# Performance work log

Hardware: AMD Instinct MI355X
Metric: run time of the kernel (lower is better)

Reference implementation:

```python
import jax, jax.numpy as jnp
import numpy as np

KNN = 5            # module constant KNN
MAX_STEPS = 100    # laplacian_optimization default
BOUND_LAMBDA = 1.0 # laplacian_optimization default


def setup_inputs() -> dict:
    key = jax.random.key(0)
    k1, k2, k3 = jax.random.split(key, 3)
    N, D, C = 4096, 2048, 256
    x = jax.random.normal(k1, (N, D), dtype=jnp.float32)          # pooled backbone features
    W = jax.random.normal(k2, (C, D), dtype=jnp.float32) * 0.02   # classifier weight
    b = jax.random.normal(k3, (C,), dtype=jnp.float32) * 0.02     # classifier bias
    return {"x": x, "W": W, "b": b}


def _rbf_affinity(feats, knn):
    # pairwise euclidean distances via gram matrix (torch.cdist equivalent)
    sq = jnp.sum(feats * feats, axis=-1)
    d2 = jnp.maximum(sq[:, None] + sq[None, :] - 2.0 * (feats @ feats.T), 0.0)
    dist = jnp.sqrt(d2)
    # k-th smallest distance per row (self-distance included, matching torch.topk largest=False)
    kth = -jax.lax.top_k(-dist, knn)[0][:, -1]
    sigma = jnp.mean(kth)
    return jnp.exp(-d2 / (2.0 * sigma * sigma))


def _laplacian_optimization(unary, kernel):
    Y0 = jax.nn.softmax(-unary, axis=-1)

    def step(carry, i):
        Y, oldE, done = carry
        pairwise = BOUND_LAMBDA * (kernel @ Y)                      # [N,N]@[N,C]
        Ynew = jax.nn.softmax(-unary + pairwise, axis=-1)
        E = jnp.sum(unary * Ynew - BOUND_LAMBDA * pairwise * Ynew
                    + Ynew * jnp.log(jnp.clip(Ynew, 1e-20)))
        conv = (i > 1) & (jnp.abs(E - oldE) <= 1e-8 * jnp.abs(oldE))
        # freeze state after convergence (device-side analogue of the host .item() break)
        Yk = jnp.where(done, Y, Ynew)
        Ek = jnp.where(done, oldE, E)
        return (Yk, Ek, done | conv), None

    init = (Y0, jnp.array(jnp.inf, jnp.float32), jnp.array(False))
    (Y, _, _), _ = jax.lax.scan(step, init, jnp.arange(MAX_STEPS))
    return Y


def reference(x, W, b):
    logits = x @ W.T + b
    unary = -jnp.log(jax.nn.softmax(logits, axis=-1) + 1e-10)
    feats = x / jnp.linalg.norm(x, axis=-1, keepdims=True)          # F.normalize(p=2)
    kernel = _rbf_affinity(feats, KNN)
    return _laplacian_optimization(unary, kernel)
```

## Files before the change

kernel.cpp:

```cpp
#include <hip/hip_runtime.h>
#include <cstdint>

#define NP 4096
#define DIMF 2048
#define NC 256
#define MAXIT 100
#define NBLK2 256

typedef __bf16 bf16x8 __attribute__((ext_vector_type(8)));
typedef float f32x4 __attribute__((ext_vector_type(4)));

__device__ inline unsigned short f2b(float f) {
  union { float f; unsigned u; } v; v.f = f;
  unsigned r = v.u + 0x7fffu + ((v.u >> 16) & 1u);
  return (unsigned short)(r >> 16);
}
__device__ inline float b2f(unsigned short u) {
  union { unsigned u; float f; } v; v.u = ((unsigned)u) << 16;
  return v.f;
}

__device__ __forceinline__ void g2lds16(const void* g, void* l) {
  __builtin_amdgcn_global_load_lds(
      (const __attribute__((address_space(1))) unsigned int*)g,
      (__attribute__((address_space(3))) unsigned int*)l, 16, 0, 0);
}

__device__ __forceinline__ void gridbar(unsigned* flags, unsigned* gen,
                                        unsigned phase, int tid, int nblk) {
  __syncthreads();
  if (blockIdx.x == 0) {
    if (tid >= 1 && tid < nblk) {
      while (__hip_atomic_load(&flags[tid * 32], __ATOMIC_ACQUIRE,
                               __HIP_MEMORY_SCOPE_AGENT) < phase)
        __builtin_amdgcn_s_sleep(1);
    }
    __syncthreads();
    if (tid == 0)
      __hip_atomic_store(gen, phase, __ATOMIC_RELEASE, __HIP_MEMORY_SCOPE_AGENT);
  } else {
    if (tid == 0) {
      __hip_atomic_store(&flags[blockIdx.x * 32], phase, __ATOMIC_RELEASE,
                         __HIP_MEMORY_SCOPE_AGENT);
      while (__hip_atomic_load(gen, __ATOMIC_ACQUIRE,
                               __HIP_MEMORY_SCOPE_AGENT) < phase)
        __builtin_amdgcn_s_sleep(1);
    }
  }
  __syncthreads();
}

__global__ __launch_bounds__(256) void initk(double* Ed, float* sig,
                                             unsigned* flags, unsigned* gen) {
  int t = threadIdx.x;
  if (t < MAXIT) Ed[t] = 0.0;
  if (t == 0) { *sig = 0.0f; *gen = 0u; }
  for (int i = t; i < NBLK2 * 32; i += 256) flags[i] = 0u;
}

__global__ __launch_bounds__(256) void castk(const float* __restrict__ W,
                                             unsigned short* __restrict__ Wb) {
  size_t i = ((size_t)blockIdx.x * 256 + threadIdx.x) * 4;
  float4 v = *(const float4*)&W[i];
  ushort4 o; o.x = f2b(v.x); o.y = f2b(v.y); o.z = f2b(v.z); o.w = f2b(v.w);
  *(ushort4*)&Wb[i] = o;
}

__global__ __launch_bounds__(256) void rownorm(const float* __restrict__ x,
                                               unsigned short* __restrict__ F,
                                               unsigned short* __restrict__ xb,
                                               float* __restrict__ sqF) {
  const int row = blockIdx.x, tid = threadIdx.x;
  const float* rp = x + (size_t)row * DIMF;
  float4 a = *(const float4*)&rp[tid * 8];
  float4 b = *(const float4*)&rp[tid * 8 + 4];
  float f[8] = {a.x, a.y, a.z, a.w, b.x, b.y, b.z, b.w};
  float s = 0.f;
#pragma unroll
  for (int k = 0; k < 8; k++) s += f[k] * f[k];
  __shared__ float red[256];
  red[tid] = s; __syncthreads();
  for (int st = 128; st >= 1; st >>= 1) {
    if (tid < st) red[tid] += red[tid + st];
    __syncthreads();
  }
  float inv = 1.0f / sqrtf(red[0]);
  __syncthreads();
  unsigned short fb[8], xbv[8];
  float s2 = 0.f;
#pragma unroll
  for (int k = 0; k < 8; k++) {
    fb[k] = f2b(f[k] * inv);
    xbv[k] = f2b(f[k]);
    float q = b2f(fb[k]);
    s2 += q * q;
  }
  *(ushort4*)&F[(size_t)row * DIMF + tid * 8]      = *(ushort4*)&fb[0];
  *(ushort4*)&F[(size_t)row * DIMF + tid * 8 + 4]  = *(ushort4*)&fb[4];
  *(ushort4*)&xb[(size_t)row * DIMF + tid * 8]     = *(ushort4*)&xbv[0];
  *(ushort4*)&xb[(size_t)row * DIMF + tid * 8 + 4] = *(ushort4*)&xbv[4];
  red[tid] = s2; __syncthreads();
  for (int st = 128; st >= 1; st >>= 1) {
    if (tid < st) red[tid] += red[tid + st];
    __syncthreads();
  }
  if (tid == 0) sqF[row] = red[0];
}

template <int BM, int BN, int EPI>
__global__ __launch_bounds__(256) void gemm2(const unsigned short* __restrict__ A,
                                             const unsigned short* __restrict__ B,
                                             float* __restrict__ C,
                                             int M, int N, int K,
                                             const float* __restrict__ aux) {
  constexpr int TM = BM / 32, TN = BN / 32;
  __shared__ __align__(16) unsigned short sA[BM * 32];
  __shared__ __align__(16) unsigned short sB[BN * 32];
  const int tid = threadIdx.x, lane = tid & 63, wid = tid >> 6;
  const int wr = wid >> 1, wc = wid & 1;
  const int l15 = lane & 15, l16 = lane >> 4;
  const int bm = blockIdx.x * BM, bn = blockIdx.y * BN;
  f32x4 acc[TM][TN];
#pragma unroll
  for (int m = 0; m < TM; m++)
#pragma unroll
    for (int n = 0; n < TN; n++) acc[m][n] = 0.0f;

  for (int k0 = 0; k0 < K; k0 += 32) {
#pragma unroll
    for (int j = 0; j < BM / 64; ++j) {
      int u = j * 256 + tid, r = u >> 2, c = u & 3;
      g2lds16(&A[(size_t)(bm + r) * K + k0 + c * 8], &sA[u * 8]);
    }
#pragma unroll
    for (int j = 0; j < BN / 64; ++j) {
      int u = j * 256 + tid, r = u >> 2, c = u & 3;
      g2lds16(&B[(size_t)(bn + r) * K + k0 + c * 8], &sB[u * 8]);
    }
    __syncthreads();
    bf16x8 af[TM], bf[TN];
#pragma unroll
    for (int m = 0; m < TM; m++)
      af[m] = *(const bf16x8*)&sA[(wr * TM * 16 + m * 16 + l15) * 32 + l16 * 8];
#pragma unroll
    for (int n = 0; n < TN; n++)
      bf[n] = *(const bf16x8*)&sB[(wc * TN * 16 + n * 16 + l15) * 32 + l16 * 8];
#pragma unroll
    for (int m = 0; m < TM; m++)
#pragma unroll
      for (int n = 0; n < TN; n++)
        acc[m][n] = __builtin_amdgcn_mfma_f32_16x16x32_bf16(af[m], bf[n], acc[m][n], 0, 0, 0);
    __syncthreads();
  }
#pragma unroll
  for (int m = 0; m < TM; m++) {
    int row0 = bm + wr * TM * 16 + m * 16 + l16 * 4;
#pragma unroll
    for (int n = 0; n < TN; n++) {
      int col = bn + wc * TN * 16 + n * 16 + l15;
#pragma unroll
      for (int j = 0; j < 4; j++) {
        int row = row0 + j;
        float v = acc[m][n][j];
        if (EPI == 0) {
          C[(size_t)row * N + col] = v + aux[col];
        } else {
          float d = aux[row] + aux[col] - 2.0f * v;
          C[(size_t)row * N + col] = fmaxf(d, 0.0f);
        }
      }
    }
  }
}

__global__ __launch_bounds__(256) void unary_k(const float* __restrict__ logits,
                                               float* __restrict__ unary) {
  const int wid = threadIdx.x >> 6, lane = threadIdx.x & 63;
  const int row = blockIdx.x * 4 + wid;
  const float* lp = logits + (size_t)row * NC;
  float v[4];
#pragma unroll
  for (int j = 0; j < 4; j++) v[j] = lp[lane + 64 * j];
  float m = fmaxf(fmaxf(v[0], v[1]), fmaxf(v[2], v[3]));
#pragma unroll
  for (int o = 32; o >= 1; o >>= 1) m = fmaxf(m, __shfl_xor(m, o, 64));
  float e[4], s = 0.f;
#pragma unroll
  for (int j = 0; j < 4; j++) { e[j] = expf(v[j] - m); s += e[j]; }
#pragma unroll
  for (int o = 32; o >= 1; o >>= 1) s += __shfl_xor(s, o, 64);
  float* up = unary + (size_t)row * NC;
#pragma unroll
  for (int j = 0; j < 4; j++) up[lane + 64 * j] = -logf(e[j] / s + 1e-10f);
}


__global__ __launch_bounds__(256) void smax0(const float* __restrict__ unary,
                                             float* __restrict__ Yout,
                                             unsigned short* __restrict__ Yt) {
  const int tid = threadIdx.x;
  const int wid = tid >> 6, lane = tid & 63;
  const int rb = blockIdx.x;
  __shared__ __align__(16) unsigned short yt[256][24];
  for (int rr = wid; rr < 16; rr += 4) {
    const int row = rb * 16 + rr;
    float z[4];
#pragma unroll
    for (int j = 0; j < 4; j++) z[j] = -unary[(size_t)row * NC + lane + 64 * j];
    float m = fmaxf(fmaxf(z[0], z[1]), fmaxf(z[2], z[3]));
#pragma unroll
    for (int o = 32; o >= 1; o >>= 1) m = fmaxf(m, __shfl_xor(m, o, 64));
    float e[4], s = 0.f;
#pragma unroll
    for (int j = 0; j < 4; j++) { e[j] = expf(z[j] - m); s += e[j]; }
#pragma unroll
    for (int o = 32; o >= 1; o >>= 1) s += __shfl_xor(s, o, 64);
#pragma unroll
    for (int j = 0; j < 4; j++) {
      int c = lane + 64 * j;
      float y = e[j] / s;
      Yout[(size_t)row * NC + c] = y;
      yt[c][rr] = f2b(y);
    }
  }
  __syncthreads();
  const int c = tid;
#pragma unroll
  for (int r8 = 0; r8 < 2; ++r8) {
    unsigned v[4];
#pragma unroll
    for (int k = 0; k < 4; ++k) {
      unsigned lo = yt[c][r8 * 8 + 2 * k];
      unsigned hi = yt[c][r8 * 8 + 2 * k + 1];
      v[k] = lo | (hi << 16);
    }
    size_t off = ((size_t)(c >> 5) << 17) +
                 (size_t)(((rb * 2 + r8) * 32 + (c & 31)) * 8);
    *(uint4*)&Yt[off] = make_uint4(v[0], v[1], v[2], v[3]);
  }
}

__global__ __launch_bounds__(256) void kth_k(const float* __restrict__ d2,
                                             float* __restrict__ sig) {
  const int row = blockIdx.x, tid = threadIdx.x;
  const float* rp = d2 + (size_t)row * NP;
  float b[5];
#pragma unroll
  for (int q = 0; q < 5; q++) b[q] = __int_as_float(0x7f800000);
  for (int s = 0; s < 16; s++) {
    float v = rp[tid + 256 * s];
    if (v < b[4]) {
      b[4] = v;
#pragma unroll
      for (int q = 4; q > 0; q--)
        if (b[q] < b[q - 1]) { float t = b[q]; b[q] = b[q - 1]; b[q - 1] = t; }
    }
  }
  __shared__ float ls[256 * 5];
#pragma unroll
  for (int q = 0; q < 5; q++) ls[tid * 5 + q] = b[q];
  __syncthreads();
  for (int st = 128; st >= 1; st >>= 1) {
    if (tid < st) {
      float* xs = &ls[tid * 5];
      float* ys = &ls[(tid + st) * 5];
      float r[5]; int i = 0, j = 0;
#pragma unroll
      for (int q = 0; q < 5; q++) r[q] = (xs[i] <= ys[j]) ? xs[i++] : ys[j++];
#pragma unroll
      for (int q = 0; q < 5; q++) xs[q] = r[q];
    }
    __syncthreads();
  }
  if (tid == 0) atomicAdd(sig, sqrtf(ls[4]));
}

__global__ __launch_bounds__(256) void expk(const float* __restrict__ d2,
                                            unsigned short* __restrict__ Kb,
                                            const float* __restrict__ sig) {
  float sigma = (*sig) * (1.0f / NP);
  float c = -1.0f / (2.0f * sigma * sigma);
  size_t i = ((size_t)blockIdx.x * 256 + threadIdx.x) * 4;
  float4 v = *(const float4*)&d2[i];
  ushort4 o;
  o.x = f2b(expf(v.x * c)); o.y = f2b(expf(v.y * c));
  o.z = f2b(expf(v.z * c)); o.w = f2b(expf(v.w * c));
  *(ushort4*)&Kb[i] = o;
}

__global__ __launch_bounds__(512) void loop_k(const unsigned short* __restrict__ Kb,
                                              unsigned short* __restrict__ Yt0,
                                              unsigned short* __restrict__ Yt1,
                                              const float* __restrict__ unary,
                                              float* __restrict__ out,
                                              double* __restrict__ Ed,
                                              unsigned* __restrict__ flags,
                                              unsigned* __restrict__ gen) {
  const int tid = threadIdx.x, lane = tid & 63, wid = tid >> 6;
  const int blk = blockIdx.x;
  const int R0 = blk * 16;
  const int l15 = lane & 15, l16 = lane >> 4;
  constexpr int LDA = 520;
  constexpr int LDP = 260;
  constexpr int LDY = 258;
  __shared__ __align__(16) unsigned short sA[2][16 * LDA];
  __shared__ __align__(16) float P[16 * LDP];
  __shared__ __align__(16) unsigned short yt[16 * LDY];
  __shared__ double ered[8];
  float oldEf = __int_as_float(0x7f800000);

  const int b0 = l15 * 8;
  const int b1 = (16 + l15) * 8;
  const int sr0 = tid >> 6, sc0 = tid & 63;
  const int sr1 = (512 + tid) >> 6, sc1 = tid & 63;

  for (int iter = 0; iter < MAXIT; ++iter) {
    const unsigned short* Yrd = ((iter & 1) ? Yt1 : Yt0) + ((size_t)wid << 17);
    unsigned short* Ywr = (iter & 1) ? Yt0 : Yt1;

    f32x4 acc[2];
    acc[0] = 0.0f; acc[1] = 0.0f;

    uint4 pre0 = *(const uint4*)&Kb[(size_t)(R0 + sr0) * NP + sc0 * 8];
    uint4 pre1 = *(const uint4*)&Kb[(size_t)(R0 + sr1) * NP + sc1 * 8];
    bf16x8 qa[2][2], qb[2][2], cb[2][2];
    qa[0][0] = *(const bf16x8*)&Yrd[(size_t)(0 + l16) * 256 + b0];
    qa[0][1] = *(const bf16x8*)&Yrd[(size_t)(4 + l16) * 256 + b0];
    qa[1][0] = *(const bf16x8*)&Yrd[(size_t)(0 + l16) * 256 + b1];
    qa[1][1] = *(const bf16x8*)&Yrd[(size_t)(4 + l16) * 256 + b1];
    qb[0][0] = *(const bf16x8*)&Yrd[(size_t)(8 + l16) * 256 + b0];
    qb[0][1] = *(const bf16x8*)&Yrd[(size_t)(12 + l16) * 256 + b0];
    qb[1][0] = *(const bf16x8*)&Yrd[(size_t)(8 + l16) * 256 + b1];
    qb[1][1] = *(const bf16x8*)&Yrd[(size_t)(12 + l16) * 256 + b1];

    for (int ch = 0; ch < 8; ++ch) {
      unsigned short* buf = sA[ch & 1];
      *(uint4*)&buf[sr0 * LDA + sc0 * 8] = pre0;
      *(uint4*)&buf[sr1 * LDA + sc1 * 8] = pre1;
      __syncthreads();
      if (ch < 7) {
        pre0 = *(const uint4*)&Kb[(size_t)(R0 + sr0) * NP + (ch + 1) * 512 + sc0 * 8];
        pre1 = *(const uint4*)&Kb[(size_t)(R0 + sr1) * NP + (ch + 1) * 512 + sc1 * 8];
      }
#pragma unroll
      for (int sub = 0; sub < 8; ++sub) {
#pragma unroll
        for (int n = 0; n < 2; ++n)
#pragma unroll
          for (int kk = 0; kk < 2; ++kk) { cb[n][kk] = qa[n][kk]; qa[n][kk] = qb[n][kk]; }
        {
          int kq = ch * 64 + sub * 8 + 16;
          if (kq > 504) kq = 504;
          qb[0][0] = *(const bf16x8*)&Yrd[(size_t)(kq + l16) * 256 + b0];
          qb[0][1] = *(const bf16x8*)&Yrd[(size_t)(kq + 4 + l16) * 256 + b0];
          qb[1][0] = *(const bf16x8*)&Yrd[(size_t)(kq + l16) * 256 + b1];
          qb[1][1] = *(const bf16x8*)&Yrd[(size_t)(kq + 4 + l16) * 256 + b1];
        }
        bf16x8 af[2];
        af[0] = *(const bf16x8*)&buf[l15 * LDA + sub * 64 + l16 * 8];
        af[1] = *(const bf16x8*)&buf[l15 * LDA + sub * 64 + 32 + l16 * 8];
#pragma unroll
        for (int kk = 0; kk < 2; ++kk)
#pragma unroll
          for (int n = 0; n < 2; ++n)
            acc[n] = __builtin_amdgcn_mfma_f32_16x16x32_bf16(af[kk], cb[n][kk], acc[n], 0, 0, 0);
      }
      __syncthreads();
    }
#pragma unroll
    for (int n = 0; n < 2; ++n)
#pragma unroll
      for (int j = 0; j < 4; ++j)
        P[(l16 * 4 + j) * LDP + wid * 32 + n * 16 + l15] = acc[n][j];
    __syncthreads();

    double ep = 0.0;
#pragma unroll
    for (int h = 0; h < 2; ++h) {
      const int r = wid * 2 + h;
      const int row = R0 + r;
      const int c0 = lane * 4;
      float4 p4 = *(const float4*)&P[r * LDP + c0];
      float pv[4] = {p4.x, p4.y, p4.z, p4.w};
      float4 u4 = *(const float4*)&unary[(size_t)row * NC + c0];
      float uu[4] = {u4.x, u4.y, u4.z, u4.w};
      float z[4];
#pragma unroll
      for (int q = 0; q < 4; ++q) z[q] = pv[q] - uu[q];
      float m = fmaxf(fmaxf(z[0], z[1]), fmaxf(z[2], z[3]));
#pragma unroll
      for (int o = 32; o >= 1; o >>= 1) m = fmaxf(m, __shfl_xor(m, o, 64));
      float e[4], ssum = 0.f;
#pragma unroll
      for (int q = 0; q < 4; ++q) { e[q] = expf(z[q] - m); ssum += e[q]; }
#pragma unroll
      for (int o = 32; o >= 1; o >>= 1) ssum += __shfl_xor(ssum, o, 64);
      float inv = 1.0f / ssum;
      float y[4];
#pragma unroll
      for (int q = 0; q < 4; ++q) {
        y[q] = e[q] * inv;
        ep += (double)(y[q] * (uu[q] - pv[q] + logf(fmaxf(y[q], 1e-20f))));
        yt[r * LDY + c0 + q] = f2b(y[q]);
      }
      float4 o4; o4.x = y[0]; o4.y = y[1]; o4.z = y[2]; o4.w = y[3];
      *(float4*)&out[(size_t)row * NC + c0] = o4;
    }
#pragma unroll
    for (int o = 32; o >= 1; o >>= 1) ep += __shfl_xor(ep, o, 64);
    if (lane == 0) ered[wid] = ep;
    __syncthreads();

    {
      const int c = tid & 255, r8 = tid >> 8;
      unsigned v[4];
#pragma unroll
      for (int k = 0; k < 4; ++k) {
        unsigned lo = yt[(r8 * 8 + 2 * k) * LDY + c];
        unsigned hi = yt[(r8 * 8 + 2 * k + 1) * LDY + c];
        v[k] = lo | (hi << 16);
      }
      size_t off = ((size_t)(c >> 5) << 17) +
                   (size_t)(((blk * 2 + r8) * 32 + (c & 31)) * 8);
      *(uint4*)&Ywr[off] = make_uint4(v[0], v[1], v[2], v[3]);
    }
    if (tid == 0) {
      double eblk = 0.0;
#pragma unroll
      for (int w = 0; w < 8; ++w) eblk += ered[w];
      atomicAdd(&Ed[iter], eblk);
    }
    gridbar(flags, gen, (unsigned)(iter + 1), tid, NBLK2);

    double Ec = __hip_atomic_load(&Ed[iter], __ATOMIC_RELAXED, __HIP_MEMORY_SCOPE_AGENT);
    float Ef = (float)Ec;
    if (iter > 1 && fabsf(Ef - oldEf) <= 1e-8f * fabsf(oldEf)) break;
    oldEf = Ef;
  }
}

extern "C" void kernel_launch(void* const* d_in, const int* in_sizes, int n_in,
                              void* d_out, int out_size, void* d_ws, size_t ws_size,
                              hipStream_t stream) {
  const float* x = (const float*)d_in[0];
  const float* W = (const float*)d_in[1];
  const float* bias = (const float*)d_in[2];
  float* out = (float*)d_out;

  char* p = (char*)d_ws;
  auto take = [&](size_t bytes) {
    char* r = p;
    p += (bytes + 255) & ~(size_t)255;
    return r;
  };
  float* d2          = (float*)take((size_t)NP * NP * 4);
  unsigned short* Kb = (unsigned short*)take((size_t)NP * NP * 2);
  unsigned short* F  = (unsigned short*)take((size_t)NP * DIMF * 2);
  unsigned short* xb = (unsigned short*)take((size_t)NP * DIMF * 2);
  unsigned short* Wb = (unsigned short*)take((size_t)NC * DIMF * 2);
  unsigned short* Yt0 = (unsigned short*)take((size_t)NC * NP * 2);
  unsigned short* Yt1 = (unsigned short*)take((size_t)NC * NP * 2);
  float* logits = (float*)take((size_t)NP * NC * 4);
  float* unary  = (float*)take((size_t)NP * NC * 4);
  float* sqF    = (float*)take((size_t)NP * 4);
  float* sig    = (float*)take(256);
  double* Ed    = (double*)take(MAXIT * 8);
  unsigned* flags = (unsigned*)take((size_t)NBLK2 * 32 * 4);
  unsigned* gen   = (unsigned*)take(256);

  initk<<<1, 256, 0, stream>>>(Ed, sig, flags, gen);
  castk<<<512, 256, 0, stream>>>(W, Wb);
  rownorm<<<NP, 256, 0, stream>>>(x, F, xb, sqF);
  gemm2<64, 64, 0><<<dim3(64, 4), 256, 0, stream>>>(xb, Wb, logits, NP, NC, DIMF, bias);
  unary_k<<<1024, 256, 0, stream>>>(logits, unary);
  smax0<<<256, 256, 0, stream>>>(unary, out, Yt0);
  gemm2<128, 128, 1><<<dim3(32, 32), 256, 0, stream>>>(F, F, d2, NP, NP, DIMF, sqF);
  kth_k<<<NP, 256, 0, stream>>>(d2, sig);
  expk<<<16384, 256, 0, stream>>>(d2, Kb, sig);
  loop_k<<<NBLK2, 512, 0, stream>>>(Kb, Yt0, Yt1, unary, out, Ed, flags, gen);
}
```

Measured before the change: 557.3 us.

## Retile persistent Laplacian loop into 32-row by 128-column blocks with global exchange

Each block of the persistent iteration kernel now computes a 32-row by 128-column tile of K@Y instead of a 16-row by 256-column tile. Each Y column slab read from global memory is now reused across 32 kernel rows, which halves Y traffic per block, while each block loads twice as many K rows into shared memory. The partial products are written to a global scratch buffer (reusing the d2 region), and an extra grid barrier per iteration is added so each block can then run softmax over full 256-wide rows. The cost is a second grid-wide barrier and a global round trip for the pairwise matrix on every iteration.

```diff
diff --git a/kernel.cpp b/kernel.cpp
--- a/kernel.cpp
+++ b/kernel.cpp
@@ -293,36 +293,39 @@
                                               unsigned short* __restrict__ Yt1,
                                               const float* __restrict__ unary,
                                               float* __restrict__ out,
+                                              float* __restrict__ Pg,
                                               double* __restrict__ Ed,
                                               unsigned* __restrict__ flags,
                                               unsigned* __restrict__ gen) {
   const int tid = threadIdx.x, lane = tid & 63, wid = tid >> 6;
   const int blk = blockIdx.x;
-  const int R0 = blk * 16;
+  const int rb = blk >> 1, cs = blk & 1;
+  const int R0 = rb * 32;
+  const int rw = wid >> 2, cw = wid & 3;
   const int l15 = lane & 15, l16 = lane >> 4;
   constexpr int LDA = 520;
-  constexpr int LDP = 260;
   constexpr int LDY = 258;
-  __shared__ __align__(16) unsigned short sA[2][16 * LDA];
-  __shared__ __align__(16) float P[16 * LDP];
+  __shared__ __align__(16) unsigned short sA[2][32 * LDA];
   __shared__ __align__(16) unsigned short yt[16 * LDY];
   __shared__ double ered[8];
   float oldEf = __int_as_float(0x7f800000);
 
   const int b0 = l15 * 8;
   const int b1 = (16 + l15) * 8;
-  const int sr0 = tid >> 6, sc0 = tid & 63;
-  const int sr1 = (512 + tid) >> 6, sc1 = tid & 63;
+  const int sr[4] = {tid >> 6, (512 + tid) >> 6, (1024 + tid) >> 6, (1536 + tid) >> 6};
+  const int sc = tid & 63;
 
   for (int iter = 0; iter < MAXIT; ++iter) {
-    const unsigned short* Yrd = ((iter & 1) ? Yt1 : Yt0) + ((size_t)wid << 17);
+    const unsigned short* Yrd = ((iter & 1) ? Yt1 : Yt0) + ((size_t)(cs * 4 + cw) << 17);
     unsigned short* Ywr = (iter & 1) ? Yt0 : Yt1;
 
     f32x4 acc[2];
     acc[0] = 0.0f; acc[1] = 0.0f;
 
-    uint4 pre0 = *(const uint4*)&Kb[(size_t)(R0 + sr0) * NP + sc0 * 8];
-    uint4 pre1 = *(const uint4*)&Kb[(size_t)(R0 + sr1) * NP + sc1 * 8];
+    uint4 pre[4];
+#pragma unroll
+    for (int j = 0; j < 4; ++j)
+      pre[j] = *(const uint4*)&Kb[(size_t)(R0 + sr[j]) * NP + sc * 8];
     bf16x8 qa[2][2], qb[2][2], cb[2][2];
     qa[0][0] = *(const bf16x8*)&Yrd[(size_t)(0 + l16) * 256 + b0];
     qa[0][1] = *(const bf16x8*)&Yrd[(size_t)(4 + l16) * 256 + b0];
@@ -335,12 +338,14 @@
 
     for (int ch = 0; ch < 8; ++ch) {
       unsigned short* buf = sA[ch & 1];
-      *(uint4*)&buf[sr0 * LDA + sc0 * 8] = pre0;
-      *(uint4*)&buf[sr1 * LDA + sc1 * 8] = pre1;
+#pragma unroll
+      for (int j = 0; j < 4; ++j)
+        *(uint4*)&buf[sr[j] * LDA + sc * 8] = pre[j];
       __syncthreads();
       if (ch < 7) {
-        pre0 = *(const uint4*)&Kb[(size_t)(R0 + sr0) * NP + (ch + 1) * 512 + sc0 * 8];
-        pre1 = *(const uint4*)&Kb[(size_t)(R0 + sr1) * NP + (ch + 1) * 512 + sc1 * 8];
+#pragma unroll
+        for (int j = 0; j < 4; ++j)
+          pre[j] = *(const uint4*)&Kb[(size_t)(R0 + sr[j]) * NP + (ch + 1) * 512 + sc * 8];
       }
 #pragma unroll
       for (int sub = 0; sub < 8; ++sub) {
@@ -357,8 +362,8 @@
           qb[1][1] = *(const bf16x8*)&Yrd[(size_t)(kq + 4 + l16) * 256 + b1];
         }
         bf16x8 af[2];
-        af[0] = *(const bf16x8*)&buf[l15 * LDA + sub * 64 + l16 * 8];
-        af[1] = *(const bf16x8*)&buf[l15 * LDA + sub * 64 + 32 + l16 * 8];
+        af[0] = *(const bf16x8*)&buf[(rw * 16 + l15) * LDA + sub * 64 + l16 * 8];
+        af[1] = *(const bf16x8*)&buf[(rw * 16 + l15) * LDA + sub * 64 + 32 + l16 * 8];
 #pragma unroll
         for (int kk = 0; kk < 2; ++kk)
 #pragma unroll
@@ -371,16 +376,17 @@
     for (int n = 0; n < 2; ++n)
 #pragma unroll
       for (int j = 0; j < 4; ++j)
-        P[(l16 * 4 + j) * LDP + wid * 32 + n * 16 + l15] = acc[n][j];
-    __syncthreads();
+        Pg[(size_t)(R0 + rw * 16 + l16 * 4 + j) * NC + cs * 128 + cw * 32 + n * 16 + l15] =
+            acc[n][j];
+    gridbar(flags, gen, 2u * iter + 1u, tid, NBLK2);
 
     double ep = 0.0;
 #pragma unroll
     for (int h = 0; h < 2; ++h) {
       const int r = wid * 2 + h;
-      const int row = R0 + r;
+      const int row = R0 + cs * 16 + r;
       const int c0 = lane * 4;
-      float4 p4 = *(const float4*)&P[r * LDP + c0];
+      float4 p4 = *(const float4*)&Pg[(size_t)row * NC + c0];
       float pv[4] = {p4.x, p4.y, p4.z, p4.w};
       float4 u4 = *(const float4*)&unary[(size_t)row * NC + c0];
       float uu[4] = {u4.x, u4.y, u4.z, u4.w};
@@ -420,8 +426,9 @@
         unsigned hi = yt[(r8 * 8 + 2 * k + 1) * LDY + c];
         v[k] = lo | (hi << 16);
       }
+      const int k8 = rb * 4 + cs * 2 + r8;
       size_t off = ((size_t)(c >> 5) << 17) +
-                   (size_t)(((blk * 2 + r8) * 32 + (c & 31)) * 8);
+                   (size_t)((k8 * 32 + (c & 31)) * 8);
       *(uint4*)&Ywr[off] = make_uint4(v[0], v[1], v[2], v[3]);
     }
     if (tid == 0) {
@@ -430,7 +437,7 @@
       for (int w = 0; w < 8; ++w) eblk += ered[w];
       atomicAdd(&Ed[iter], eblk);
     }
-    gridbar(flags, gen, (unsigned)(iter + 1), tid, NBLK2);
+    gridbar(flags, gen, 2u * iter + 2u, tid, NBLK2);
 
     double Ec = __hip_atomic_load(&Ed[iter], __ATOMIC_RELAXED, __HIP_MEMORY_SCOPE_AGENT);
     float Ef = (float)Ec;
@@ -467,6 +474,7 @@
   double* Ed    = (double*)take(MAXIT * 8);
   unsigned* flags = (unsigned*)take((size_t)NBLK2 * 32 * 4);
   unsigned* gen   = (unsigned*)take(256);
+  float* Pg = d2;
 
   initk<<<1, 256, 0, stream>>>(Ed, sig, flags, gen);
   castk<<<512, 256, 0, stream>>>(W, Wb);
@@ -477,5 +485,5 @@
   gemm2<128, 128, 1><<<dim3(32, 32), 256, 0, stream>>>(F, F, d2, NP, NP, DIMF, sqF);
   kth_k<<<NP, 256, 0, stream>>>(d2, sig);
   expk<<<16384, 256, 0, stream>>>(d2, Kb, sig);
-  loop_k<<<NBLK2, 512, 0, stream>>>(Kb, Yt0, Yt1, unary, out, Ed, flags, gen);
-}
+  loop_k<<<NBLK2, 512, 0, stream>>>(Kb, Yt0, Yt1, unary, out, Pg, Ed, flags, gen);
+}
```

After: 830.5 us. 1.49x slower.
